# Performance work log

Measured on AMD Instinct MI355X. Metric: run time of the kernel, lower is better.

The kernel has to match this reference:

```python
import jax, jax.numpy as jnp
import numpy as np

NUM_HEADS = 4
HEAD_DIM = 128  # out_dim // num_heads = 512 // 4
TOP_K = 16
NEG_SLOPE = 0.2


def setup_inputs() -> dict:
    key = jax.random.key(0)
    k1, k2, k3, k4 = jax.random.split(key, 4)
    N, in_dim, out_dim = 4096, 1024, 512
    x = jax.random.normal(k1, (N, in_dim), dtype=jnp.float32)
    adj = jax.random.uniform(k2, (N, N), dtype=jnp.float32)  # all-positive, like softmax attn
    W = jax.random.normal(k3, (out_dim, in_dim), dtype=jnp.float32) * 0.02
    a = jax.random.normal(k4, (1, 2 * HEAD_DIM), dtype=jnp.float32) * 0.02
    return {"x": x, "adj": adj, "W": W, "a": a}


def reference(x, adj, W, a):
    N = x.shape[0]
    Wh = (x @ W.T).reshape(N, NUM_HEADS, HEAD_DIM)  # (N, H, D)

    # _sparsify_adj: keep top-k per row, binary mask
    k = min(TOP_K, N)
    _, topk_idx = jax.lax.top_k(adj, k)  # (N, k)
    rows = jnp.arange(N)[:, None]
    sparse = jnp.zeros_like(adj).at[rows, topk_idx].set(1.0)
    mask = sparse > 0  # (N_i, N_j)

    # a([Wh_i, Wh_j]) decomposed: a = [a_src | a_dst], score = s_i + s_j
    a_src, a_dst = a[0, :HEAD_DIM], a[0, HEAD_DIM:]
    s_i = jnp.einsum("nhd,d->nh", Wh, a_src)  # (N, H)
    s_j = jnp.einsum("nhd,d->nh", Wh, a_dst)  # (N, H)
    e = jax.nn.leaky_relu(s_i[:, None, :] + s_j[None, :, :], NEG_SLOPE)  # (N_i, N_j, H)
    e = jnp.where(mask[:, :, None], e, -jnp.inf)

    alpha = jax.nn.softmax(e, axis=1)  # softmax over neighbors j
    alpha = jnp.nan_to_num(alpha, nan=0.0)

    out = jnp.einsum("imh,mhd->ihd", alpha, Wh)  # weighted sum over j
    return jax.nn.elu(out.reshape(N, -1))  # (N, out_dim)
```

## Files before the change

### kernel.cpp

```cpp
#include <hip/hip_runtime.h>
#include <hip/hip_bf16.h>

#define N_NODES 4096
#define IN_DIM 1024
#define OUT_DIM 512
#define NUM_HEADS 4
#define HEAD_DIM 128
#define TOP_K 16
#define NEG_SLOPE 0.2f

typedef __attribute__((ext_vector_type(8))) short bf16x8;
typedef __attribute__((ext_vector_type(4))) float f32x4;

typedef __attribute__((address_space(3))) unsigned as3_u32;
typedef const __attribute__((address_space(1))) unsigned as1_u32;

static __device__ __forceinline__ void gld16(const void* g, void* l) {
    __builtin_amdgcn_global_load_lds((as1_u32*)g, (as3_u32*)l, 16, 0, 0);
}

__device__ __forceinline__ unsigned short f2bf(float f) {
    unsigned u = __float_as_uint(f);
    unsigned r = u + 0x7FFFu + ((u >> 16) & 1u);
    return (unsigned short)(r >> 16);
}
__device__ __forceinline__ float bf2f(unsigned short h) {
    return __uint_as_float(((unsigned)h) << 16);
}

__device__ __forceinline__ void conv_row(const float* __restrict__ src,
                                         unsigned short* __restrict__ dst, int t)
{
    int row = t >> 7, rem = t & 127, kb = rem >> 2, c = rem & 3;
    const float* s = src + (size_t)row * IN_DIM + kb * 32 + c * 8;
    float4 v0 = *(const float4*)s;
    float4 v1 = *(const float4*)(s + 4);
    float vv[8] = {v0.x, v0.y, v0.z, v0.w, v1.x, v1.y, v1.z, v1.w};
    bf16x8 H, L;
#pragma unroll
    for (int e = 0; e < 8; ++e) {
        unsigned short h = f2bf(vv[e]);
        H[e] = (short)h;
        L[e] = (short)f2bf(vv[e] - bf2f(h));
    }
    int sw = row & 7;
    unsigned short* base = dst + (size_t)row * 2048 + kb * 64;
    *(bf16x8*)(base + ((c ^ sw) << 3))       = H;
    *(bf16x8*)(base + (((c + 4) ^ sw) << 3)) = L;
}

__global__ __launch_bounds__(256) void prep_kernel(
    const float* __restrict__ x, const float* __restrict__ W,
    unsigned short* __restrict__ xc, unsigned short* __restrict__ wc,
    float* __restrict__ szero)
{
    int b = blockIdx.x, tid = threadIdx.x;
    if (b < 2048) {
        conv_row(x, xc, b * 256 + tid);
    } else if (b < 2304) {
        conv_row(W, wc, (b - 2048) * 256 + tid);
    } else {
        int t = (b - 2304) * 256 + tid;
        ((float4*)szero)[t] = (float4){0.f, 0.f, 0.f, 0.f};
    }
}

#define GBM 128
#define GBN 64

__global__ __launch_bounds__(256) void gemm_kernel(
    const unsigned short* __restrict__ xc, const unsigned short* __restrict__ wc,
    const float* __restrict__ a, unsigned short* __restrict__ Whb,
    float* __restrict__ s_src, float* __restrict__ s_dst)
{
    __shared__ __align__(16) unsigned short A0[GBM * 64];
    __shared__ __align__(16) unsigned short A1[GBM * 64];
    __shared__ __align__(16) unsigned short A2[GBM * 64];
    __shared__ __align__(16) unsigned short B0[GBN * 64];
    __shared__ __align__(16) unsigned short B1[GBN * 64];
    __shared__ __align__(16) unsigned short B2[GBN * 64];

    const int tid = threadIdx.x;
    const int id  = blockIdx.x;
    const int xcd = id & 7, seq = id >> 3;
    const int bm  = xcd * 4 + (seq >> 3), bn = seq & 7;

    const int wave = tid >> 6, lane = tid & 63;
    const int wm = wave >> 1, wn = wave & 1;
    const int lr = lane & 15, lk = lane >> 4;

    f32x4 acc[4][2];
#pragma unroll
    for (int i = 0; i < 4; ++i)
#pragma unroll
        for (int j = 0; j < 2; ++j) acc[i][j] = (f32x4){0.f, 0.f, 0.f, 0.f};

#define STAGE(Abuf, Bbuf, kt) do {                                            \
        size_t koff = (size_t)(kt) * 128;                                     \
        _Pragma("unroll")                                                     \
        for (int q = 0; q < 4; ++q) {             \
            int ci = q * 256 + tid;                                           \
            int row = ci >> 3, p = ci & 7;                                    \
            gld16((const char*)xc + ((size_t)(bm * GBM + row) * 4096 + koff + p * 16), \
                  (char*)(Abuf) + (size_t)ci * 16);                           \
        }                                                                     \
        _Pragma("unroll")                                                     \
        for (int q = 0; q < 2; ++q) {               \
            int ci = q * 256 + tid;                                           \
            int row = ci >> 3, p = ci & 7;                                    \
            gld16((const char*)wc + ((size_t)(bn * GBN + row) * 4096 + koff + p * 16), \
                  (char*)(Bbuf) + (size_t)ci * 16);                           \
        }                                                                     \
    } while (0)

#define COMPUTE(Abuf, Bbuf) do {                                              \
        bf16x8 bh[2], bl[2];                                                  \
        _Pragma("unroll")                                                     \
        for (int ni = 0; ni < 2; ++ni) {                                      \
            int rb = wn * 32 + ni * 16 + lr; int swb = rb & 7;                \
            bh[ni] = *(const bf16x8*)&(Bbuf)[rb * 64 + ((lk ^ swb) << 3)];    \
            bl[ni] = *(const bf16x8*)&(Bbuf)[rb * 64 + (((4 + lk) ^ swb) << 3)]; \
        }                                                                     \
        __builtin_amdgcn_s_setprio(1);                                        \
        _Pragma("unroll")                                                     \
        for (int mi = 0; mi < 4; ++mi) {                                      \
            int r = wm * 64 + mi * 16 + lr; int sw = r & 7;                   \
            bf16x8 ah = *(const bf16x8*)&(Abuf)[r * 64 + ((lk ^ sw) << 3)];   \
            bf16x8 al = *(const bf16x8*)&(Abuf)[r * 64 + (((4 + lk) ^ sw) << 3)]; \
            _Pragma("unroll")                                                 \
            for (int ni = 0; ni < 2; ++ni) {                                  \
                acc[mi][ni] = __builtin_amdgcn_mfma_f32_16x16x32_bf16(ah, bh[ni], acc[mi][ni], 0, 0, 0); \
                acc[mi][ni] = __builtin_amdgcn_mfma_f32_16x16x32_bf16(ah, bl[ni], acc[mi][ni], 0, 0, 0); \
                acc[mi][ni] = __builtin_amdgcn_mfma_f32_16x16x32_bf16(al, bh[ni], acc[mi][ni], 0, 0, 0); \
            }                                                                 \
        }                                                                     \
        __builtin_amdgcn_s_setprio(0);                                        \
    } while (0)

#define BODY(Ac, Bc, An, Bn, ktn, W) do {                                     \
        asm volatile("s_waitcnt vmcnt(" #W ")" ::: "memory");                 \
        __builtin_amdgcn_s_barrier();                                         \
        asm volatile("" ::: "memory");                                        \
        if ((ktn) < 32) STAGE(An, Bn, ktn);                                   \
        COMPUTE(Ac, Bc);                                                      \
    } while (0)

    STAGE(A0, B0, 0);
    STAGE(A1, B1, 1);

    for (int i = 0; i < 10; ++i) {
        int t = i * 3;
        BODY(A0, B0, A2, B2, t + 2, 6);
        BODY(A1, B1, A0, B0, t + 3, 6);
        BODY(A2, B2, A1, B1, t + 4, 6);
    }
    BODY(A0, B0, A2, B2, 32, 6);
    asm volatile("s_waitcnt vmcnt(0)" ::: "memory");
    __builtin_amdgcn_s_barrier();
    asm volatile("" ::: "memory");
    COMPUTE(A1, B1);

#undef BODY
#undef COMPUTE
#undef STAGE

    const int h = bn >> 1;
    float ca[2], cb[2];
#pragma unroll
    for (int ni = 0; ni < 2; ++ni) {
        int dcol = (bn & 1) * 64 + wn * 32 + ni * 16 + lr;
        ca[ni] = a[dcol];
        cb[ni] = a[HEAD_DIM + dcol];
    }
#pragma unroll
    for (int mi = 0; mi < 4; ++mi) {
        float ss[4] = {0.f, 0.f, 0.f, 0.f}, sd[4] = {0.f, 0.f, 0.f, 0.f};
#pragma unroll
        for (int ni = 0; ni < 2; ++ni) {
            int col_g = bn * GBN + wn * 32 + ni * 16 + lr;
#pragma unroll
            for (int r = 0; r < 4; ++r) {
                int row_g = bm * GBM + wm * 64 + mi * 16 + lk * 4 + r;
                float v = acc[mi][ni][r];
                Whb[(size_t)row_g * OUT_DIM + col_g] = f2bf(v);
                ss[r] += v * ca[ni];
                sd[r] += v * cb[ni];
            }
        }
#pragma unroll
        for (int s = 1; s < 16; s <<= 1)
#pragma unroll
            for (int r = 0; r < 4; ++r) {
                ss[r] += __shfl_xor(ss[r], s);
                sd[r] += __shfl_xor(sd[r], s);
            }
        if (lr == 0) {
#pragma unroll
            for (int r = 0; r < 4; ++r) {
                int row_g = bm * GBM + wm * 64 + mi * 16 + lk * 4 + r;
                atomicAdd(&s_src[row_g * NUM_HEADS + h], ss[r]);
                atomicAdd(&s_dst[row_g * NUM_HEADS + h], sd[r]);
            }
        }
    }
}

#define TK_THRESH 0.988f
#define TK_CAP 128

__global__ __launch_bounds__(256) void topk_kernel(
    const float* __restrict__ adj, int* __restrict__ topk)
{
    const int wave = threadIdx.x >> 6, lane = threadIdx.x & 63;
    const int row  = blockIdx.x * 4 + wave;
    const float* rp = adj + (size_t)row * N_NODES;
    __shared__ unsigned long long cand[4][TK_CAP];

    float v[64];
#pragma unroll
    for (int i = 0; i < 16; ++i) {
        float4 q = *(const float4*)(rp + i * 256 + lane * 4);
        v[i * 4 + 0] = q.x; v[i * 4 + 1] = q.y; v[i * 4 + 2] = q.z; v[i * 4 + 3] = q.w;
    }
    int* op = topk + (size_t)row * TOP_K;

    const unsigned long long lmask = (1ull << lane) - 1ull;
    int cnt = 0;
#pragma unroll
    for (int s = 0; s < 64; ++s) {
        int g = (s >> 2) * 256 + lane * 4 + (s & 3);
        bool p = v[s] >= TK_THRESH;
        unsigned long long m = __ballot(p);
        if (p) {
            int pos = cnt + __popcll(m & lmask);
            if (pos < TK_CAP) {
                unsigned b  = __float_as_uint(v[s]);
                unsigned mo = b ^ (unsigned)(((int)b >> 31) | 0x80000000);
                cand[wave][pos] =
                    ((unsigned long long)mo << 32) | (unsigned)(N_NODES - 1 - g);
            }
        }
        cnt += __popcll(m);
    }

    if (cnt >= TOP_K && cnt <= TK_CAP) {
        for (int j = cnt + lane; j < TK_CAP; j += 64) cand[wave][j] = 0ull;
        unsigned long long c0 = cand[wave][lane], c1 = cand[wave][lane + 64];
        for (int r = 0; r < TOP_K; ++r) {
            unsigned long long b = c0 > c1 ? c0 : c1;
#pragma unroll
            for (int m = 1; m < 64; m <<= 1) {
                unsigned long long o = __shfl_xor(b, m);
                b = o > b ? o : b;
            }
            if (lane == 0) op[r] = N_NODES - 1 - (int)(unsigned)(b & 0xFFFFFFFFu);
            if (c0 == b) c0 = 0ull;
            if (c1 == b) c1 = 0ull;
        }
    } else {
        for (int r = 0; r < TOP_K; ++r) {
            float bv = -INFINITY; int bg = 0x7fffffff;
#pragma unroll
            for (int s = 0; s < 64; ++s) {
                int g = (s >> 2) * 256 + lane * 4 + (s & 3);
                bool better = (v[s] > bv) || (v[s] == bv && g < bg);
                bv = better ? v[s] : bv;
                bg = better ? g : bg;
            }
#pragma unroll
            for (int m = 1; m < 64; m <<= 1) {
                float ov = __shfl_xor(bv, m);
                int   og = __shfl_xor(bg, m);
                bool better = (ov > bv) || (ov == bv && og < bg);
                bv = better ? ov : bv;
                bg = better ? og : bg;
            }
            if (lane == 0) op[r] = bg;
#pragma unroll
            for (int s = 0; s < 64; ++s) {
                int g = (s >> 2) * 256 + lane * 4 + (s & 3);
                if (g == bg) v[s] = -INFINITY;
            }
        }
    }
}

__global__ __launch_bounds__(256) void aggregate_kernel(
    const unsigned short* __restrict__ Whb, const int* __restrict__ topk,
    const float* __restrict__ s_src, const float* __restrict__ s_dst,
    float* __restrict__ out)
{
    const int i = blockIdx.x, t = threadIdx.x;
    __shared__ int   sidx[TOP_K];
    __shared__ float salpha[TOP_K][NUM_HEADS];
    __shared__ float part[3][8][64];

    if (t < 64) {
        int idxv = 0;
        if (t < TOP_K) { idxv = topk[(size_t)i * TOP_K + t]; sidx[t] = idxv; }
        int m = t >> 2, h = t & 3;
        int im = __shfl(idxv, m);
        float e = s_src[i * NUM_HEADS + h] + s_dst[im * NUM_HEADS + h];
        e = (e >= 0.f) ? e : NEG_SLOPE * e;
        float mx = e;
#pragma unroll
        for (int s = 4; s < 64; s <<= 1) mx = fmaxf(mx, __shfl_xor(mx, s));
        float ex = expf(e - mx);
        float sum = ex;
#pragma unroll
        for (int s = 4; s < 64; s <<= 1) sum += __shfl_xor(sum, s);
        salpha[m][h] = ex / sum;
    }
    __syncthreads();

    const int g = t >> 6, o = t & 63;
    const int h = o >> 4;
    float acc8[8] = {0.f, 0.f, 0.f, 0.f, 0.f, 0.f, 0.f, 0.f};
#pragma unroll
    for (int q = 0; q < 4; ++q) {
        int m = g * 4 + q;
        float al = salpha[m][h];
        bf16x8 v = *(const bf16x8*)&Whb[(size_t)sidx[m] * OUT_DIM + o * 8];
#pragma unroll
        for (int e = 0; e < 8; ++e)
            acc8[e] += al * bf2f((unsigned short)v[e]);
    }
    if (g) {
#pragma unroll
        for (int e = 0; e < 8; ++e) part[g - 1][e][o] = acc8[e];
    }
    __syncthreads();
    if (!g) {
        float r8[8];
#pragma unroll
        for (int e = 0; e < 8; ++e) {
            float s = acc8[e] + part[0][e][o] + part[1][e][o] + part[2][e][o];
            r8[e] = s > 0.f ? s : expf(s) - 1.f;
        }
        float4 lo = (float4){r8[0], r8[1], r8[2], r8[3]};
        float4 hi = (float4){r8[4], r8[5], r8[6], r8[7]};
        *(float4*)(out + (size_t)i * OUT_DIM + o * 8)     = lo;
        *(float4*)(out + (size_t)i * OUT_DIM + o * 8 + 4) = hi;
    }
}

extern "C" void kernel_launch(void* const* d_in, const int* in_sizes, int n_in,
                              void* d_out, int out_size, void* d_ws, size_t ws_size,
                              hipStream_t stream) {
    const float* x   = (const float*)d_in[0];
    const float* adj = (const float*)d_in[1];
    const float* W   = (const float*)d_in[2];
    const float* a   = (const float*)d_in[3];
    float* out = (float*)d_out;

    char* ws = (char*)d_ws;
    unsigned short* Whb   = (unsigned short*)ws;
    unsigned short* xc    = (unsigned short*)(ws + (8u << 20));
    unsigned short* wc    = (unsigned short*)(ws + (24u << 20));
    float*          s_src = (float*)(ws + (26u << 20));
    float*          s_dst = s_src + N_NODES * NUM_HEADS;
    int*            topkb = (int*)(s_dst + N_NODES * NUM_HEADS);

    prep_kernel<<<2336, 256, 0, stream>>>(x, W, xc, wc, s_src);
    gemm_kernel<<<256, 256, 0, stream>>>(xc, wc, a, Whb, s_src, s_dst);
    topk_kernel<<<N_NODES / 4, 256, 0, stream>>>(adj, topkb);
    aggregate_kernel<<<N_NODES, 256, 0, stream>>>(Whb, topkb, s_src, s_dst, out);
}
```

Before: 158.2 us.

## Split each top-k row across four waves with shared-memory candidate merge

The top-k kernel now assigns one row per 256-thread block instead of one row per wave. Each wave filters a quarter of the row against the threshold into its own candidate list, and wave 0 merges the four lists. The fallback path stages the row in shared memory and runs selection from there. This cuts registers per thread (16 floats instead of 64) and the serial filter length, raising memory-level parallelism, at the cost of a block barrier and 16KB of LDS per block.

Result: no change. 159.3 us (+0.7%).

```diff
diff --git a/kernel.cpp b/kernel.cpp
--- a/kernel.cpp
+++ b/kernel.cpp
@@ -206,80 +206,107 @@
 }
 
 #define TK_THRESH 0.988f
-#define TK_CAP 128
 
 __global__ __launch_bounds__(256) void topk_kernel(
     const float* __restrict__ adj, int* __restrict__ topk)
 {
-    const int wave = threadIdx.x >> 6, lane = threadIdx.x & 63;
-    const int row  = blockIdx.x * 4 + wave;
+    const int row  = blockIdx.x;
+    const int tid  = threadIdx.x;
+    const int wave = tid >> 6, lane = tid & 63;
     const float* rp = adj + (size_t)row * N_NODES;
-    __shared__ unsigned long long cand[4][TK_CAP];
-
-    float v[64];
-#pragma unroll
-    for (int i = 0; i < 16; ++i) {
-        float4 q = *(const float4*)(rp + i * 256 + lane * 4);
-        v[i * 4 + 0] = q.x; v[i * 4 + 1] = q.y; v[i * 4 + 2] = q.z; v[i * 4 + 3] = q.w;
-    }
-    int* op = topk + (size_t)row * TOP_K;
+
+    __shared__ unsigned long long cand[4][64];
+    __shared__ int wcnt[4];
+    __shared__ float srow[N_NODES];
+
+    float4 q0 = *(const float4*)(rp + wave * 1024 + 0 * 256 + lane * 4);
+    float4 q1 = *(const float4*)(rp + wave * 1024 + 1 * 256 + lane * 4);
+    float4 q2 = *(const float4*)(rp + wave * 1024 + 2 * 256 + lane * 4);
+    float4 q3 = *(const float4*)(rp + wave * 1024 + 3 * 256 + lane * 4);
 
     const unsigned long long lmask = (1ull << lane) - 1ull;
     int cnt = 0;
-#pragma unroll
-    for (int s = 0; s < 64; ++s) {
-        int g = (s >> 2) * 256 + lane * 4 + (s & 3);
-        bool p = v[s] >= TK_THRESH;
-        unsigned long long m = __ballot(p);
-        if (p) {
-            int pos = cnt + __popcll(m & lmask);
-            if (pos < TK_CAP) {
-                unsigned b  = __float_as_uint(v[s]);
-                unsigned mo = b ^ (unsigned)(((int)b >> 31) | 0x80000000);
-                cand[wave][pos] =
-                    ((unsigned long long)mo << 32) | (unsigned)(N_NODES - 1 - g);
-            }
-        }
-        cnt += __popcll(m);
-    }
-
-    if (cnt >= TOP_K && cnt <= TK_CAP) {
-        for (int j = cnt + lane; j < TK_CAP; j += 64) cand[wave][j] = 0ull;
-        unsigned long long c0 = cand[wave][lane], c1 = cand[wave][lane + 64];
-        for (int r = 0; r < TOP_K; ++r) {
-            unsigned long long b = c0 > c1 ? c0 : c1;
-#pragma unroll
-            for (int m = 1; m < 64; m <<= 1) {
-                unsigned long long o = __shfl_xor(b, m);
-                b = o > b ? o : b;
-            }
-            if (lane == 0) op[r] = N_NODES - 1 - (int)(unsigned)(b & 0xFFFFFFFFu);
-            if (c0 == b) c0 = 0ull;
-            if (c1 == b) c1 = 0ull;
+
+#define FILT(qv, i, e, comp) do {                                             \
+        float val = (qv).comp;                                                \
+        int g = wave * 1024 + (i) * 256 + lane * 4 + (e);                     \
+        bool p = val >= TK_THRESH;                                            \
+        unsigned long long m = __ballot(p);                                   \
+        if (p) {                                                              \
+            int pos = cnt + __popcll(m & lmask);                              \
+            if (pos < 64) {                                                   \
+                unsigned b  = __float_as_uint(val);                           \
+                unsigned mo = b ^ (unsigned)(((int)b >> 31) | 0x80000000);    \
+                cand[wave][pos] =                                             \
+                    ((unsigned long long)mo << 32) | (unsigned)(N_NODES - 1 - g); \
+            }                                                                 \
+        }                                                                     \
+        cnt += __popcll(m);                                                   \
+    } while (0)
+
+    FILT(q0, 0, 0, x); FILT(q0, 0, 1, y); FILT(q0, 0, 2, z); FILT(q0, 0, 3, w);
+    FILT(q1, 1, 0, x); FILT(q1, 1, 1, y); FILT(q1, 1, 2, z); FILT(q1, 1, 3, w);
+    FILT(q2, 2, 0, x); FILT(q2, 2, 1, y); FILT(q2, 2, 2, z); FILT(q2, 2, 3, w);
+    FILT(q3, 3, 0, x); FILT(q3, 3, 1, y); FILT(q3, 3, 2, z); FILT(q3, 3, 3, w);
+#undef FILT
+
+    if (lane == 0) wcnt[wave] = cnt;
+    __syncthreads();
+
+    const int c0n = wcnt[0], c1n = wcnt[1], c2n = wcnt[2], c3n = wcnt[3];
+    const int total = c0n + c1n + c2n + c3n;
+    const bool ok = (total >= TOP_K) &&
+                    (c0n <= 64) && (c1n <= 64) && (c2n <= 64) && (c3n <= 64);
+    int* op = topk + (size_t)row * TOP_K;
+
+    if (ok) {
+        if (wave == 0) {
+            unsigned long long k0 = lane < c0n ? cand[0][lane] : 0ull;
+            unsigned long long k1 = lane < c1n ? cand[1][lane] : 0ull;
+            unsigned long long k2 = lane < c2n ? cand[2][lane] : 0ull;
+            unsigned long long k3 = lane < c3n ? cand[3][lane] : 0ull;
+            for (int r = 0; r < TOP_K; ++r) {
+                unsigned long long a01 = k0 > k1 ? k0 : k1;
+                unsigned long long a23 = k2 > k3 ? k2 : k3;
+                unsigned long long b = a01 > a23 ? a01 : a23;
+#pragma unroll
+                for (int m = 1; m < 64; m <<= 1) {
+                    unsigned long long o = __shfl_xor(b, m);
+                    b = o > b ? o : b;
+                }
+                if (lane == 0) op[r] = N_NODES - 1 - (int)(unsigned)(b & 0xFFFFFFFFu);
+                if (k0 == b) k0 = 0ull;
+                if (k1 == b) k1 = 0ull;
+                if (k2 == b) k2 = 0ull;
+                if (k3 == b) k3 = 0ull;
+            }
         }
     } else {
-        for (int r = 0; r < TOP_K; ++r) {
-            float bv = -INFINITY; int bg = 0x7fffffff;
-#pragma unroll
-            for (int s = 0; s < 64; ++s) {
-                int g = (s >> 2) * 256 + lane * 4 + (s & 3);
-                bool better = (v[s] > bv) || (v[s] == bv && g < bg);
-                bv = better ? v[s] : bv;
-                bg = better ? g : bg;
-            }
-#pragma unroll
-            for (int m = 1; m < 64; m <<= 1) {
-                float ov = __shfl_xor(bv, m);
-                int   og = __shfl_xor(bg, m);
-                bool better = (ov > bv) || (ov == bv && og < bg);
-                bv = better ? ov : bv;
-                bg = better ? og : bg;
-            }
-            if (lane == 0) op[r] = bg;
-#pragma unroll
-            for (int s = 0; s < 64; ++s) {
-                int g = (s >> 2) * 256 + lane * 4 + (s & 3);
-                if (g == bg) v[s] = -INFINITY;
+        int base = wave * 1024 + lane * 4;
+        *(float4*)&srow[base + 0 * 256] = q0;
+        *(float4*)&srow[base + 1 * 256] = q1;
+        *(float4*)&srow[base + 2 * 256] = q2;
+        *(float4*)&srow[base + 3 * 256] = q3;
+        __syncthreads();
+        if (wave == 0) {
+            for (int r = 0; r < TOP_K; ++r) {
+                float bv = -INFINITY; int bg = 0x7fffffff;
+                for (int j = 0; j < 64; ++j) {
+                    int g = j * 64 + lane;
+                    float val = srow[g];
+                    bool better = (val > bv) || (val == bv && g < bg);
+                    bv = better ? val : bv;
+                    bg = better ? g : bg;
+                }
+#pragma unroll
+                for (int m = 1; m < 64; m <<= 1) {
+                    float ov = __shfl_xor(bv, m);
+                    int   og = __shfl_xor(bg, m);
+                    bool better = (ov > bv) || (ov == bv && og < bg);
+                    bv = better ? ov : bv;
+                    bg = better ? og : bg;
+                }
+                if (lane == 0) { op[r] = bg; srow[bg] = -INFINITY; }
             }
         }
     }
@@ -363,6 +390,6 @@
 
     prep_kernel<<<2336, 256, 0, stream>>>(x, W, xc, wc, s_src);
     gemm_kernel<<<256, 256, 0, stream>>>(xc, wc, a, Whb, s_src, s_dst);
-    topk_kernel<<<N_NODES / 4, 256, 0, stream>>>(adj, topkb);
+    topk_kernel<<<N_NODES, 256, 0, stream>>>(adj, topkb);
     aggregate_kernel<<<N_NODES, 256, 0, stream>>>(Whb, topkb, s_src, s_dst, out);
 }
```
